# Kernel tuning notes

Hardware: AMD Instinct MI355X
Metric: run time of the kernel (lower is better)

Reference implementation:

```python
import jax, jax.numpy as jnp
import numpy as np

N_NODES = 100000
N_EDGES = 3200000
F_IN, HIDDEN, N_CLASSES = 512, 256, 40


def setup_inputs() -> dict:
    key = jax.random.key(0)
    ks = jax.random.split(key, 8)
    x = jax.random.normal(ks[0], (N_NODES, F_IN), dtype=jnp.float32)
    edge_row = jax.random.randint(ks[1], (N_EDGES,), 0, N_NODES, dtype=jnp.int64)
    edge_col = jax.random.randint(ks[2], (N_EDGES,), 0, N_NODES, dtype=jnp.int64)
    edge_val = jax.random.uniform(ks[3], (N_EDGES,), dtype=jnp.float32)
    # Xavier-uniform-ish weights
    lim1 = float(np.sqrt(6.0 / (F_IN + HIDDEN)))
    lim2 = float(np.sqrt(6.0 / (HIDDEN + N_CLASSES)))
    W1 = jax.random.uniform(ks[4], (F_IN, HIDDEN), minval=-lim1, maxval=lim1, dtype=jnp.float32)
    b1 = jnp.zeros((HIDDEN,), dtype=jnp.float32)
    W2 = jax.random.uniform(ks[5], (HIDDEN, N_CLASSES), minval=-lim2, maxval=lim2, dtype=jnp.float32)
    b2 = jnp.zeros((N_CLASSES,), dtype=jnp.float32)
    return {"x": x, "edge_row": edge_row, "edge_col": edge_col, "edge_val": edge_val,
            "W1": W1, "b1": b1, "W2": W2, "b2": b2}


def _spmm(edge_row, edge_col, edge_val, h):
    # out[r] = sum_e val[e] * h[col[e]] for edges with row[e]==r  (a @ h)
    msg = edge_val[:, None] * h[edge_col]            # [E, F] gather + scale
    return jax.ops.segment_sum(msg, edge_row, num_segments=N_NODES)


def reference(x, edge_row, edge_col, edge_val, W1, b1, W2, b2):
    # Layer 1: dense mm -> spmm -> bias -> relu (dropout in eval mode = identity)
    h = _spmm(edge_row, edge_col, edge_val, x @ W1) + b1
    h = jax.nn.relu(h)
    # Layer 2: dense mm -> spmm -> bias
    logits = _spmm(edge_row, edge_col, edge_val, h @ W2) + b2
    return jax.nn.log_softmax(logits, axis=1)
```

## Files before the change

### kernel.cpp

```cpp
#include <hip/hip_runtime.h>
#include <math.h>

#define NN  100000
#define NE  3200000
#define FIN 512
#define HID 256
#define NC  40

#define NBUK 391
#define SPB  9472
#define CHUNK 4096
#define COLMASK 0x1FFFF

typedef __attribute__((ext_vector_type(8))) short short8;
typedef __attribute__((ext_vector_type(4))) float f32x4;

__device__ inline float bf2f(unsigned short u) {
    unsigned int x = ((unsigned int)u) << 16;
    return __builtin_bit_cast(float, x);
}
__device__ inline unsigned short f2bfu(float f) {
    unsigned int x = __builtin_bit_cast(unsigned int, f);
    unsigned int r = (x + 0x7fffu + ((x >> 16) & 1u)) >> 16;
    return (unsigned short)r;
}
__device__ inline signed char q8(float v, float s) {
    int q = (int)rintf(v * s);
    q = max(-127, min(127, q));
    return (signed char)q;
}
__device__ inline unsigned cvtpk_bf16(float lo, float hi) {
    unsigned r;
    asm("v_cvt_pk_bf16_f32 %0, %1, %2" : "=v"(r) : "v"(lo), "v"(hi));
    return r;
}
__device__ inline float cub0(int r) { float f; asm("v_cvt_f32_ubyte0 %0, %1" : "=v"(f) : "v"(r)); return f; }
__device__ inline float cub1(int r) { float f; asm("v_cvt_f32_ubyte1 %0, %1" : "=v"(f) : "v"(r)); return f; }
__device__ inline float cub2(int r) { float f; asm("v_cvt_f32_ubyte2 %0, %1" : "=v"(f) : "v"(r)); return f; }
__device__ inline float cub3(int r) { float f; asm("v_cvt_f32_ubyte3 %0, %1" : "=v"(f) : "v"(r)); return f; }

__global__ __launch_bounds__(256) void k_w1t(const float* __restrict__ W1, unsigned short* __restrict__ W1T) {
    int b = blockIdx.x;
    int n = threadIdx.x;
    unsigned short tmp[16];
#pragma unroll
    for (int kk = 0; kk < 16; kk++)
        tmp[kk] = f2bfu(W1[(size_t)(b * 16 + kk) * HID + n]);
    unsigned short* dst = W1T + (size_t)n * FIN + b * 16;
    *(short8*)dst = *(short8*)tmp;
    *(short8*)(dst + 8) = *(short8*)(tmp + 8);
}

__global__ __launch_bounds__(512) void k_fused(const float* __restrict__ x, const unsigned short* __restrict__ W1T,
                                               unsigned char* __restrict__ h1,
                                               const int* __restrict__ er, const int* __restrict__ ec,
                                               const float* __restrict__ ev, int* __restrict__ bcnt,
                                               int2* __restrict__ spack) {
    __shared__ __align__(16) char smem[61440];
    const int role = blockIdx.x & 1;
    const int gid = blockIdx.x >> 1;
    const int tid = threadIdx.x;

    if (role == 1) {
        int* hist = (int*)smem;
        int* lscan = (int*)(smem + 1568);
        int* gbase = (int*)(smem + 3136);
        int* lcur  = (int*)(smem + 4700);
        int* sm    = (int*)(smem + 6272);
        int2* ebuf = (int2*)(smem + 8320);
        unsigned short* bbuf = (unsigned short*)(smem + 41088);
        if (tid < 392) hist[tid] = 0;
        if (tid < 391) lcur[tid] = 0;
        __syncthreads();
        const int start = gid * CHUNK;
        const int end = min(start + CHUNK, NE);
        const int n = end - start;
        for (int e = start + tid; e < end; e += 512)
            atomicAdd(&hist[er[e] >> 8], 1);
        __syncthreads();
        int v = (tid < 392) ? hist[tid] : 0;
        sm[tid] = v;
        __syncthreads();
        for (int off = 1; off < 512; off <<= 1) {
            int t2 = (tid >= off) ? sm[tid - off] : 0;
            __syncthreads();
            sm[tid] += t2;
            __syncthreads();
        }
        if (tid < 392) lscan[tid] = sm[tid] - v;
        if (tid < 391) {
            int h = hist[tid];
            gbase[tid] = h ? atomicAdd(&bcnt[tid], h) : 0;
        }
        __syncthreads();
        for (int e = start + tid; e < end; e += 512) {
            int r = er[e];
            int bk = r >> 8;
            int lpos = atomicAdd(&lcur[bk], 1);
            int pos = lscan[bk] + lpos;
            int2 p;
            p.x = ((r & 255) << 17) | ec[e];
            p.y = __builtin_bit_cast(int, ev[e]);
            ebuf[pos] = p;
            bbuf[pos] = (unsigned short)bk;
        }
        __syncthreads();
        for (int i = tid; i < n; i += 512) {
            int bk = bbuf[i];
            spack[(size_t)bk * SPB + gbase[bk] + (i - lscan[bk])] = ebuf[i];
        }
        return;
    }

    typedef unsigned short AsT[128][40];
    typedef unsigned short BsT[256][40];
    AsT* As = (AsT*)smem;
    BsT* Bs = (BsT*)(smem + 20480);
    const int row0 = gid * 128;
    const int lane = tid & 63;
    const int w = tid >> 6;
    const int wr = (w >> 2) * 64;
    const int wc = (w & 3) * 64;
    const int m16 = lane & 15;
    const int quad = lane >> 4;

    const int arow = tid >> 2;
    const int akoff = (tid & 3) * 8;
    int gar = row0 + arow;
    if (gar >= NN) gar = NN - 1;
    const float* ax = x + (size_t)gar * FIN + akoff;
    const int brow = tid >> 1;
    const int bkoff = (tid & 1) * 16;
    const unsigned short* bw = W1T + (size_t)brow * FIN + bkoff;

    f32x4 acc[4][4];
#pragma unroll
    for (int i = 0; i < 4; i++)
#pragma unroll
        for (int j = 0; j < 4; j++) acc[i][j] = (f32x4){0.f, 0.f, 0.f, 0.f};

    float4 va0, va1;
    uint4 vb0, vb1;

#define G1_LOAD(tt)                                                        \
    {                                                                      \
        const float* ap = ax + (tt) * 32;                                  \
        va0 = *(const float4*)(ap);                                        \
        va1 = *(const float4*)(ap + 4);                                    \
        const unsigned short* bp = bw + (tt) * 32;                         \
        vb0 = *(const uint4*)(bp);                                         \
        vb1 = *(const uint4*)(bp + 8);                                     \
    }

#define G1_STORE(bf)                                                       \
    {                                                                      \
        uint4 pa;                                                          \
        pa.x = cvtpk_bf16(va0.x, va0.y);                                   \
        pa.y = cvtpk_bf16(va0.z, va0.w);                                   \
        pa.z = cvtpk_bf16(va1.x, va1.y);                                   \
        pa.w = cvtpk_bf16(va1.z, va1.w);                                   \
        *(uint4*)(&As[bf][arow][akoff]) = pa;                              \
        *(uint4*)(&Bs[bf][brow][bkoff]) = vb0;                             \
        *(uint4*)(&Bs[bf][brow][bkoff + 8]) = vb1;                         \
    }

    G1_LOAD(0)
    G1_STORE(0)
    G1_LOAD(1)
    __syncthreads();

    for (int t = 0; t < 16; ++t) {
        const int buf = t & 1;
        short8 af[4], bfr[4];
#pragma unroll
        for (int i = 0; i < 4; i++) af[i] = *(const short8*)(&As[buf][wr + i * 16 + m16][quad * 8]);
#pragma unroll
        for (int j = 0; j < 4; j++) bfr[j] = *(const short8*)(&Bs[buf][wc + j * 16 + m16][quad * 8]);
        if (t < 15) {
            G1_STORE(buf ^ 1)
            if (t < 14) G1_LOAD(t + 2)
        }
#pragma unroll
        for (int i = 0; i < 4; i++)
#pragma unroll
            for (int j = 0; j < 4; j++)
                acc[i][j] = __builtin_amdgcn_mfma_f32_16x16x32_bf16(af[i], bfr[j], acc[i][j], 0, 0, 0);
        __syncthreads();
    }
#undef G1_LOAD
#undef G1_STORE

#pragma unroll
    for (int i = 0; i < 4; i++) {
#pragma unroll
        for (int r = 0; r < 4; r++) {
            int gr = row0 + wr + i * 16 + quad * 4 + r;
            if (gr < NN) {
#pragma unroll
                for (int j = 0; j < 4; j++) {
                    int c = wc + j * 16 + m16;
                    h1[(size_t)gr * HID + c] = (unsigned char)(q8(acc[i][j][r], 16.f) + 128);
                }
            }
        }
    }
}

__global__ __launch_bounds__(256) void k_finecsr(const int2* __restrict__ spack, const int* __restrict__ bcnt,
                                                 int2* __restrict__ cpack,
                                                 int* __restrict__ row_beg, int* __restrict__ row_cnt,
                                                 const float* __restrict__ W2, unsigned short* __restrict__ W2T) {
    if (blockIdx.x >= NBUK) {
        int n = blockIdx.x - NBUK;
        int k = threadIdx.x;
        float v = (n < NC) ? W2[(size_t)k * NC + n] : 0.f;
        W2T[(size_t)n * HID + k] = f2bfu(v);
        return;
    }
    __shared__ int cnt[256];
    __shared__ int sm[256];
    __shared__ int cur[256];
    int tid = threadIdx.x;
    int buk = blockIdx.x;
    size_t bb = (size_t)buk * SPB;
    int n = min(bcnt[buk], SPB);
    cnt[tid] = 0;
    __syncthreads();
    for (int i = tid; i < n; i += 256) {
        int lr = ((unsigned)spack[bb + i].x) >> 17;
        atomicAdd(&cnt[lr], 1);
    }
    __syncthreads();
    int v = cnt[tid];
    sm[tid] = v;
    __syncthreads();
    for (int off = 1; off < 256; off <<= 1) {
        int t = (tid >= off) ? sm[tid - off] : 0;
        __syncthreads();
        sm[tid] += t;
        __syncthreads();
    }
    int ex = sm[tid] - v;
    cur[tid] = ex;
    int grow = buk * 256 + tid;
    if (grow < NN) {
        row_beg[grow] = (int)bb + ex;
        row_cnt[grow] = v;
    }
    __syncthreads();
    for (int i = tid; i < n; i += 256) {
        int2 p = spack[bb + i];
        int lr = ((unsigned)p.x) >> 17;
        int pos = atomicAdd(&cur[lr], 1);
        int2 q;
        q.x = p.x & COLMASK;
        q.y = p.y;
        cpack[bb + pos] = q;
    }
}

__global__ __launch_bounds__(256) void k_spmm1(const unsigned char* __restrict__ h1,
                                               const int2* __restrict__ cpack,
                                               const int* __restrict__ row_beg, const int* __restrict__ row_cnt,
                                               const float* __restrict__ b1, unsigned short* __restrict__ a1) {
    const int lane = threadIdx.x & 63;
    const int row = (int)__builtin_amdgcn_readfirstlane(blockIdx.x * 4 + (threadIdx.x >> 6));
    if (row >= NN) return;
    const int beg = (int)__builtin_amdgcn_readfirstlane(row_beg[row]);
    const int cnt = (int)__builtin_amdgcn_readfirstlane(row_cnt[row]);
    const int end = beg + cnt;
    const int voff = lane * 4;
    float su[4] = {0.f, 0.f, 0.f, 0.f};
    float sv = 0.f;

    for (int e0 = beg; e0 < end; e0 += 16) {
        int2 p[16];
#pragma unroll
        for (int j = 0; j < 16; j++)
            p[j] = cpack[e0 + j];
        unsigned cb[16];
        float vv[16];
#pragma unroll
        for (int j = 0; j < 16; j++) {
            cb[j] = ((unsigned)p[j].x & COLMASK) << 8;
            vv[j] = (e0 + j) < end ? __builtin_bit_cast(float, p[j].y) : 0.f;
        }
        int g[16];
#pragma unroll
        for (int j = 0; j < 16; j++)
            g[j] = *(const int*)(h1 + (size_t)cb[j] + voff);
#pragma unroll
        for (int j = 0; j < 16; j++) {
            sv += vv[j];
            su[0] = fmaf(vv[j], cub0(g[j]), su[0]);
            su[1] = fmaf(vv[j], cub1(g[j]), su[1]);
            su[2] = fmaf(vv[j], cub2(g[j]), su[2]);
            su[3] = fmaf(vv[j], cub3(g[j]), su[3]);
        }
    }

    const int col = lane * 4;
    const float4 bb = *(const float4*)(b1 + col);
    ushort4 o;
    o.x = f2bfu(fmaxf(fmaf(0.0625f, fmaf(-128.f, sv, su[0]), bb.x), 0.f));
    o.y = f2bfu(fmaxf(fmaf(0.0625f, fmaf(-128.f, sv, su[1]), bb.y), 0.f));
    o.z = f2bfu(fmaxf(fmaf(0.0625f, fmaf(-128.f, sv, su[2]), bb.z), 0.f));
    o.w = f2bfu(fmaxf(fmaf(0.0625f, fmaf(-128.f, sv, su[3]), bb.w), 0.f));
    *(ushort4*)(a1 + (size_t)row * HID + col) = o;
}

__global__ __launch_bounds__(256) void k_gemm2(const unsigned short* __restrict__ a1,
                                               const unsigned short* __restrict__ W2T, unsigned char* __restrict__ h2) {
    const int tid = threadIdx.x;
    const int lane = tid & 63;
    const int w = tid >> 6;
    const int m16 = lane & 15;
    const int quad = lane >> 4;
    const int r0 = blockIdx.x * 256 + w * 64;

    f32x4 acc[4][3];
#pragma unroll
    for (int i = 0; i < 4; i++)
#pragma unroll
        for (int j = 0; j < 3; j++) acc[i][j] = (f32x4){0.f, 0.f, 0.f, 0.f};

    for (int k0 = 0; k0 < HID; k0 += 32) {
        short8 af[4], bfr[3];
#pragma unroll
        for (int i = 0; i < 4; i++) {
            int gr = r0 + i * 16 + m16;
            if (gr >= NN) gr = NN - 1;
            af[i] = *(const short8*)(a1 + (size_t)gr * HID + k0 + quad * 8);
        }
#pragma unroll
        for (int j = 0; j < 3; j++)
            bfr[j] = *(const short8*)(W2T + (size_t)(j * 16 + m16) * HID + k0 + quad * 8);
#pragma unroll
        for (int i = 0; i < 4; i++)
#pragma unroll
            for (int j = 0; j < 3; j++)
                acc[i][j] = __builtin_amdgcn_mfma_f32_16x16x32_bf16(af[i], bfr[j], acc[i][j], 0, 0, 0);
    }
#pragma unroll
    for (int i = 0; i < 4; i++) {
#pragma unroll
        for (int r = 0; r < 4; r++) {
            int gr = r0 + i * 16 + quad * 4 + r;
            if (gr < NN) {
#pragma unroll
                for (int j = 0; j < 3; j++) {
                    int c = j * 16 + m16;
                    if (c < NC) h2[(size_t)gr * 64 + c] = (unsigned char)(q8(acc[i][j][r], 4.f) + 128);
                }
            }
        }
    }
}

__global__ __launch_bounds__(256) void k_spmm2(const unsigned char* __restrict__ h2,
                                               const int2* __restrict__ cpack,
                                               const int* __restrict__ row_beg, const int* __restrict__ row_cnt,
                                               const float* __restrict__ b2, float* __restrict__ out) {
    const int lane = threadIdx.x & 63;
    const int slot = lane >> 4;
    const int t = lane & 15;
    const int row = (int)__builtin_amdgcn_readfirstlane(blockIdx.x * 4 + (threadIdx.x >> 6));
    if (row >= NN) return;
    const int beg = (int)__builtin_amdgcn_readfirstlane(row_beg[row]);
    const int cnt = (int)__builtin_amdgcn_readfirstlane(row_cnt[row]);
    const int end = beg + cnt;
    const int t4 = t * 4;
    float su[4] = {0.f, 0.f, 0.f, 0.f};
    float sv = 0.f;

    for (int e0 = beg; e0 < end; e0 += 32) {
        unsigned cb[8];
        float vs[8];
#pragma unroll
        for (int u = 0; u < 8; u++) {
            int idx = e0 + u * 4 + slot;
            int2 p = cpack[idx];
            cb[u] = ((unsigned)p.x & COLMASK) << 6;
            vs[u] = idx < end ? __builtin_bit_cast(float, p.y) : 0.f;
        }
        int g[8];
#pragma unroll
        for (int u = 0; u < 8; u++)
            g[u] = *(const int*)(h2 + (size_t)cb[u] + t4);
#pragma unroll
        for (int u = 0; u < 8; u++) {
            sv += vs[u];
            su[0] = fmaf(vs[u], cub0(g[u]), su[0]);
            su[1] = fmaf(vs[u], cub1(g[u]), su[1]);
            su[2] = fmaf(vs[u], cub2(g[u]), su[2]);
            su[3] = fmaf(vs[u], cub3(g[u]), su[3]);
        }
    }

#pragma unroll
    for (int i = 0; i < 4; i++) {
        su[i] += __shfl_xor(su[i], 16, 64);
        su[i] += __shfl_xor(su[i], 32, 64);
    }
    sv += __shfl_xor(sv, 16, 64);
    sv += __shfl_xor(sv, 32, 64);

    const bool act = t < 10;
    const int off = t4;
    const int boff = act ? off : 0;
    const float4 bb = *(const float4*)(b2 + boff);
    float acc[4];
    acc[0] = fmaf(0.25f, fmaf(-128.f, sv, su[0]), bb.x);
    acc[1] = fmaf(0.25f, fmaf(-128.f, sv, su[1]), bb.y);
    acc[2] = fmaf(0.25f, fmaf(-128.f, sv, su[2]), bb.z);
    acc[3] = fmaf(0.25f, fmaf(-128.f, sv, su[3]), bb.w);
    float mx = act ? fmaxf(fmaxf(acc[0], acc[1]), fmaxf(acc[2], acc[3])) : -INFINITY;
#pragma unroll
    for (int o = 1; o < 16; o <<= 1) mx = fmaxf(mx, __shfl_xor(mx, o, 16));
    float se = 0.f;
    if (act) {
#pragma unroll
        for (int i = 0; i < 4; i++) se += expf(acc[i] - mx);
    }
#pragma unroll
    for (int o = 1; o < 16; o <<= 1) se += __shfl_xor(se, o, 16);
    const float ls = logf(se);
    if (act && slot == 0) {
        float4 r;
        r.x = acc[0] - mx - ls;
        r.y = acc[1] - mx - ls;
        r.z = acc[2] - mx - ls;
        r.w = acc[3] - mx - ls;
        *(float4*)(out + (size_t)row * NC + off) = r;
    }
}

extern "C" void kernel_launch(void* const* d_in, const int* in_sizes, int n_in, void* d_out, int out_size,
                              void* d_ws, size_t ws_size, hipStream_t stream) {
    const float* x  = (const float*)d_in[0];
    const int*   er = (const int*)d_in[1];
    const int*   ec = (const int*)d_in[2];
    const float* ev = (const float*)d_in[3];
    const float* W1 = (const float*)d_in[4];
    const float* b1 = (const float*)d_in[5];
    const float* W2 = (const float*)d_in[6];
    const float* b2 = (const float*)d_in[7];
    float* out = (float*)d_out;
    char* ws = (char*)d_ws;

    int2*  spack       = (int2*)(ws + 0);
    unsigned short* a1 = (unsigned short*)(ws + 0);
    unsigned char* h1  = (unsigned char*)(ws + 51200000);
    unsigned char* h2  = (unsigned char*)(ws + 76800000);
    int2*  cpack       = (int2*)(ws + 83200000);
    int*   row_beg     = (int*)(ws + 112828416);
    int*   row_cnt     = (int*)(ws + 113228416);
    int*   bcnt        = (int*)(ws + 113628416);
    unsigned short* W1T = (unsigned short*)(ws + 113630464);
    unsigned short* W2T = (unsigned short*)(ws + 113892608);

    hipMemsetAsync(bcnt, 0, NBUK * sizeof(int), stream);
    k_w1t<<<32, 256, 0, stream>>>(W1, W1T);
    k_fused<<<1564, 512, 0, stream>>>(x, W1T, h1, er, ec, ev, bcnt, spack);
    k_finecsr<<<NBUK + 48, 256, 0, stream>>>(spack, bcnt, cpack, row_beg, row_cnt, W2, W2T);
    k_spmm1<<<NN / 4, 256, 0, stream>>>(h1, cpack, row_beg, row_cnt, b1, a1);
    k_gemm2<<<(NN + 255) / 256, 256, 0, stream>>>(a1, W2T, h2);
    k_spmm2<<<NN / 4, 256, 0, stream>>>(h2, cpack, row_beg, row_cnt, b2, out);
}
```

Measured before the change: 613.4 us.

## Merge prep kernels, pad GEMM LDS tiles, and prefetch edge records in SpMM loops

The memset, the W1 transpose and the W2 transpose are folded into one prep kernel, removing a launch and a memset node. The LDS tile row stride in the fused GEMM goes from 40 to 42 halves, meant to reduce bank conflicts. Both SpMM kernels now software-prefetch the next group of packed edge records while the current gathers are in flight, hiding cpack load latency. The prefetch reads past each row's end (neighbouring rows' data or the buffer tail), and the prefetched values use more registers.

```diff
diff --git a/kernel.cpp b/kernel.cpp
--- a/kernel.cpp
+++ b/kernel.cpp
@@ -39,16 +39,26 @@
 __device__ inline float cub2(int r) { float f; asm("v_cvt_f32_ubyte2 %0, %1" : "=v"(f) : "v"(r)); return f; }
 __device__ inline float cub3(int r) { float f; asm("v_cvt_f32_ubyte3 %0, %1" : "=v"(f) : "v"(r)); return f; }
 
-__global__ __launch_bounds__(256) void k_w1t(const float* __restrict__ W1, unsigned short* __restrict__ W1T) {
-    int b = blockIdx.x;
-    int n = threadIdx.x;
-    unsigned short tmp[16];
-#pragma unroll
-    for (int kk = 0; kk < 16; kk++)
-        tmp[kk] = f2bfu(W1[(size_t)(b * 16 + kk) * HID + n]);
-    unsigned short* dst = W1T + (size_t)n * FIN + b * 16;
-    *(short8*)dst = *(short8*)tmp;
-    *(short8*)(dst + 8) = *(short8*)(tmp + 8);
+__global__ __launch_bounds__(256) void k_prep(const float* __restrict__ W1, unsigned short* __restrict__ W1T,
+                                              const float* __restrict__ W2, unsigned short* __restrict__ W2T,
+                                              int* __restrict__ bcnt) {
+    const int b = blockIdx.x;
+    const int tid = threadIdx.x;
+    if (b < 32) {
+        unsigned short tmp[16];
+#pragma unroll
+        for (int kk = 0; kk < 16; kk++)
+            tmp[kk] = f2bfu(W1[(size_t)(b * 16 + kk) * HID + tid]);
+        unsigned short* dst = W1T + (size_t)tid * FIN + b * 16;
+        *(short8*)dst = *(short8*)tmp;
+        *(short8*)(dst + 8) = *(short8*)(tmp + 8);
+    } else if (b < 80) {
+        int n = b - 32;
+        float v = (n < NC) ? W2[(size_t)tid * NC + n] : 0.f;
+        W2T[(size_t)n * HID + tid] = f2bfu(v);
+    } else {
+        for (int i = tid; i < NBUK; i += 256) bcnt[i] = 0;
+    }
 }
 
 __global__ __launch_bounds__(512) void k_fused(const float* __restrict__ x, const unsigned short* __restrict__ W1T,
@@ -56,7 +66,7 @@
                                                const int* __restrict__ er, const int* __restrict__ ec,
                                                const float* __restrict__ ev, int* __restrict__ bcnt,
                                                int2* __restrict__ spack) {
-    __shared__ __align__(16) char smem[61440];
+    __shared__ __align__(16) char smem[64512];
     const int role = blockIdx.x & 1;
     const int gid = blockIdx.x >> 1;
     const int tid = threadIdx.x;
@@ -112,10 +122,10 @@
         return;
     }
 
-    typedef unsigned short AsT[128][40];
-    typedef unsigned short BsT[256][40];
+    typedef unsigned short AsT[128][42];
+    typedef unsigned short BsT[256][42];
     AsT* As = (AsT*)smem;
-    BsT* Bs = (BsT*)(smem + 20480);
+    BsT* Bs = (BsT*)(smem + 21504);
     const int row0 = gid * 128;
     const int lane = tid & 63;
     const int w = tid >> 6;
@@ -208,15 +218,7 @@
 
 __global__ __launch_bounds__(256) void k_finecsr(const int2* __restrict__ spack, const int* __restrict__ bcnt,
                                                  int2* __restrict__ cpack,
-                                                 int* __restrict__ row_beg, int* __restrict__ row_cnt,
-                                                 const float* __restrict__ W2, unsigned short* __restrict__ W2T) {
-    if (blockIdx.x >= NBUK) {
-        int n = blockIdx.x - NBUK;
-        int k = threadIdx.x;
-        float v = (n < NC) ? W2[(size_t)k * NC + n] : 0.f;
-        W2T[(size_t)n * HID + k] = f2bfu(v);
-        return;
-    }
+                                                 int* __restrict__ row_beg, int* __restrict__ row_cnt) {
     __shared__ int cnt[256];
     __shared__ int sm[256];
     __shared__ int cur[256];
@@ -273,11 +275,12 @@
     float su[4] = {0.f, 0.f, 0.f, 0.f};
     float sv = 0.f;
 
+    int2 p[16];
+#pragma unroll
+    for (int j = 0; j < 16; j++)
+        p[j] = cpack[beg + j];
+
     for (int e0 = beg; e0 < end; e0 += 16) {
-        int2 p[16];
-#pragma unroll
-        for (int j = 0; j < 16; j++)
-            p[j] = cpack[e0 + j];
         unsigned cb[16];
         float vv[16];
 #pragma unroll
@@ -289,6 +292,9 @@
 #pragma unroll
         for (int j = 0; j < 16; j++)
             g[j] = *(const int*)(h1 + (size_t)cb[j] + voff);
+#pragma unroll
+        for (int j = 0; j < 16; j++)
+            p[j] = cpack[e0 + 16 + j];
 #pragma unroll
         for (int j = 0; j < 16; j++) {
             sv += vv[j];
@@ -373,20 +379,27 @@
     float su[4] = {0.f, 0.f, 0.f, 0.f};
     float sv = 0.f;
 
+    int2 p[8];
+#pragma unroll
+    for (int u = 0; u < 8; u++)
+        p[u] = cpack[beg + u * 4 + slot];
+
     for (int e0 = beg; e0 < end; e0 += 32) {
         unsigned cb[8];
         float vs[8];
 #pragma unroll
         for (int u = 0; u < 8; u++) {
             int idx = e0 + u * 4 + slot;
-            int2 p = cpack[idx];
-            cb[u] = ((unsigned)p.x & COLMASK) << 6;
-            vs[u] = idx < end ? __builtin_bit_cast(float, p.y) : 0.f;
+            cb[u] = ((unsigned)p[u].x & COLMASK) << 6;
+            vs[u] = idx < end ? __builtin_bit_cast(float, p[u].y) : 0.f;
         }
         int g[8];
 #pragma unroll
         for (int u = 0; u < 8; u++)
             g[u] = *(const int*)(h2 + (size_t)cb[u] + t4);
+#pragma unroll
+        for (int u = 0; u < 8; u++)
+            p[u] = cpack[e0 + 32 + u * 4 + slot];
 #pragma unroll
         for (int u = 0; u < 8; u++) {
             sv += vs[u];
@@ -459,10 +472,9 @@
     unsigned short* W1T = (unsigned short*)(ws + 113630464);
     unsigned short* W2T = (unsigned short*)(ws + 113892608);
 
-    hipMemsetAsync(bcnt, 0, NBUK * sizeof(int), stream);
-    k_w1t<<<32, 256, 0, stream>>>(W1, W1T);
+    k_prep<<<81, 256, 0, stream>>>(W1, W1T, W2, W2T, bcnt);
     k_fused<<<1564, 512, 0, stream>>>(x, W1T, h1, er, ec, ev, bcnt, spack);
-    k_finecsr<<<NBUK + 48, 256, 0, stream>>>(spack, bcnt, cpack, row_beg, row_cnt, W2, W2T);
+    k_finecsr<<<NBUK, 256, 0, stream>>>(spack, bcnt, cpack, row_beg, row_cnt);
     k_spmm1<<<NN / 4, 256, 0, stream>>>(h1, cpack, row_beg, row_cnt, b1, a1);
     k_gemm2<<<(NN + 255) / 256, 256, 0, stream>>>(a1, W2T, h2);
     k_spmm2<<<NN / 4, 256, 0, stream>>>(h2, cpack, row_beg, row_cnt, b2, out);
```

Result: slower. 735.8 us (+20.0%).
